# Kernel tuning notes

Measured on AMD Instinct MI355X. Metric: run time of the kernel, lower is better.

## Reference

```python
import jax, jax.numpy as jnp
import numpy as np

V, NJ, NCOMP, NBETA = 778, 16, 24, 10
F_CLOSED, N_ANCHOR = 1554, 32
B, NOBJ = 8, 16384
# MANO kinematic tree parents (wrist + 5 fingers x 3 joints)
PARENTS = np.array([-1, 0, 1, 2, 0, 4, 5, 0, 7, 8, 0, 10, 11, 0, 13, 14])


def setup_inputs() -> dict:
    key = jax.random.key(0)
    ks = jax.random.split(key, 12)
    hand_pose = jax.random.normal(ks[0], (B, 3 + 3 + NCOMP), jnp.float32) * 0.1
    obj_points = jax.random.normal(ks[1], (B, NOBJ, 3), jnp.float32) * 0.1
    hand_beta = jax.random.normal(ks[2], (B, NBETA), jnp.float32) * 0.5
    v_template = jax.random.normal(ks[3], (V, 3), jnp.float32) * 0.05
    shapedirs = jax.random.normal(ks[4], (V, 3, NBETA), jnp.float32) * 0.01
    posedirs = jax.random.normal(ks[5], (V, 3, (NJ - 1) * 9), jnp.float32) * 0.01
    J_regressor = jax.nn.softmax(jax.random.normal(ks[6], (NJ, V), jnp.float32), axis=-1)
    lbs_weights = jax.nn.softmax(jax.random.normal(ks[7], (V, NJ), jnp.float32) * 2.0, axis=-1)
    pca_comps = jax.random.normal(ks[8], (NCOMP, (NJ - 1) * 3), jnp.float32) * 0.1
    anchor_weights = jax.nn.softmax(jax.random.normal(ks[9], (N_ANCHOR, 3), jnp.float32), axis=-1)
    closed_faces = jax.random.randint(ks[10], (F_CLOSED, 3), 0, V, jnp.int32)
    anchor_face_idx = jax.random.randint(ks[11], (N_ANCHOR, 3), 0, V, jnp.int32)
    return dict(hand_pose=hand_pose, obj_points=obj_points, hand_beta=hand_beta,
                v_template=v_template, shapedirs=shapedirs, posedirs=posedirs,
                J_regressor=J_regressor, lbs_weights=lbs_weights, pca_comps=pca_comps,
                anchor_weights=anchor_weights, closed_faces=closed_faces,
                anchor_face_idx=anchor_face_idx)


def rodrigues(r):
    # r: [..., 3] axis-angle -> [..., 3, 3] rotation matrix
    theta = jnp.sqrt(jnp.sum(r * r, axis=-1, keepdims=True) + 1e-16)
    k = r / theta
    c = jnp.cos(theta)[..., None]
    s = jnp.sin(theta)[..., None]
    kx, ky, kz = k[..., 0], k[..., 1], k[..., 2]
    zero = jnp.zeros_like(kx)
    K = jnp.stack([zero, -kz, ky, kz, zero, -kx, -ky, kx, zero], axis=-1)
    K = K.reshape(r.shape[:-1] + (3, 3))
    I = jnp.eye(3, dtype=r.dtype)
    return c * I + s * K + (1.0 - c) * k[..., :, None] * k[..., None, :]


def mano_verts(hand_pose, hand_beta, v_template, shapedirs, posedirs,
               J_regressor, lbs_weights, pca_comps):
    b = hand_pose.shape[0]
    trans = hand_pose[:, :3]
    root = hand_pose[:, 3:6]
    hand45 = hand_pose[:, 6:] @ pca_comps  # PCA -> 45-dim pose (flat_hand_mean: no mean add)
    full = jnp.concatenate([root, hand45], axis=-1).reshape(b, NJ, 3)
    R = rodrigues(full)  # [B,16,3,3]
    v_shaped = v_template + jnp.einsum('vdk,bk->bvd', shapedirs, hand_beta)
    J = jnp.einsum('jv,bvd->bjd', J_regressor, v_shaped)  # [B,16,3]
    pose_feat = (R[:, 1:] - jnp.eye(3, dtype=R.dtype)).reshape(b, (NJ - 1) * 9)
    v_posed = v_shaped + jnp.einsum('vdp,bp->bvd', posedirs, pose_feat)

    def make44(Rj, tj):  # [B,3,3],[B,3] -> [B,4,4]
        T = jnp.zeros((b, 4, 4), R.dtype)
        return T.at[:, :3, :3].set(Rj).at[:, :3, 3].set(tj).at[:, 3, 3].set(1.0)

    Ts = [make44(R[:, 0], J[:, 0])]
    for j in range(1, NJ):  # fixed small kinematic chain
        p = int(PARENTS[j])
        Ts.append(jnp.einsum('bmn,bnk->bmk', Ts[p], make44(R[:, j], J[:, j] - J[:, p])))
    T = jnp.stack(Ts, axis=1)  # [B,16,4,4] global joint transforms
    corr = jnp.einsum('bjmn,bjn->bjm', T[..., :3, :3], J)
    A = T.at[..., :3, 3].add(-corr)  # relative-to-rest transforms
    Tw = jnp.einsum('vj,bjmn->bvmn', lbs_weights, A)  # per-vertex skinning transform
    verts = jnp.einsum('bvmn,bvn->bvm', Tw[..., :3, :3], v_posed) + Tw[..., :3, 3]
    return verts + trans[:, None, :]


def vertex_normals(verts, faces):  # verts [B,V,3], faces [F,3]
    def one(v):
        p0, p1, p2 = v[faces[:, 0]], v[faces[:, 1]], v[faces[:, 2]]
        fn = jnp.cross(p1 - p0, p2 - p0)
        vn = (jnp.zeros_like(v).at[faces[:, 0]].add(fn)
              .at[faces[:, 1]].add(fn).at[faces[:, 2]].add(fn))
        return vn / (jnp.linalg.norm(vn, axis=-1, keepdims=True) + 1e-8)
    return jax.vmap(one)(verts)


def reference(hand_pose, obj_points, hand_beta, v_template, shapedirs, posedirs,
              J_regressor, lbs_weights, pca_comps, anchor_weights,
              closed_faces, anchor_face_idx):
    verts = mano_verts(hand_pose, hand_beta, v_template, shapedirs, posedirs,
                       J_regressor, lbs_weights, pca_comps)  # [B,778,3]
    # get_NN: squared cdist obj->hand + argmin (the memory-bound bottleneck)
    d2 = (jnp.sum(obj_points * obj_points, -1, keepdims=True)
          + jnp.sum(verts * verts, -1)[:, None, :]
          - 2.0 * jnp.einsum('bnd,bvd->bnv', obj_points, verts))  # [B,NOBJ,778]
    nn_idx = jnp.argmin(d2, axis=-1)  # [B,NOBJ]
    nn_dist = jnp.take_along_axis(d2, nn_idx[..., None], axis=-1)[..., 0]
    # contact_map_of_m_to_n
    cmap = 1.0 - 2.0 * (jax.nn.sigmoid(100.0 * nn_dist) - 0.5)
    # inter_penetr_loss: interior obj points (behind nearest hand vertex normal)
    normals = vertex_normals(verts, closed_faces)
    nn_vert = jnp.take_along_axis(verts, nn_idx[..., None], axis=1)
    nn_norm = jnp.take_along_axis(normals, nn_idx[..., None], axis=1)
    interior = jnp.sum((nn_vert - obj_points) * nn_norm, axis=-1) > 0.0
    penetration = jnp.sum(jnp.where(interior, nn_dist, 0.0)) / hand_pose.shape[0]
    # AnchorLayer: barycentric anchor points on the hand surface
    contact_candidates = jnp.einsum('ak,bakd->bad', anchor_weights, verts[:, anchor_face_idx])
    return cmap, penetration, verts, contact_candidates
```

## Files before the change

kernel.cpp:

```cpp
#include <hip/hip_runtime.h>
#include <math.h>

#define NV 778
#define NJ 16
#define NCOMP 24
#define NBETA 10
#define FC 1554
#define NA 32
#define NB 8
#define NOBJ 16384
#define VD (NV*3)
#define BCH 584
#define NVQ 832
#define NG 104
#define NCB 132

__global__ __launch_bounds__(256) void k_blend(
    const float* __restrict__ hp, const float* __restrict__ pca,
    const float* __restrict__ vt, const float* __restrict__ sd,
    const float* __restrict__ pd, const float* __restrict__ beta,
    const float* __restrict__ Jreg,
    float* __restrict__ VP, float* __restrict__ C0, float* __restrict__ C1,
    float* __restrict__ pen)
{
    int bid = blockIdx.x;
    int t = threadIdx.x;
    int wid = t >> 6, lane = t & 63;

    if (bid >= NB*BCH) {
        int o = (bid - NB*BCH)*4 + wid;
        if (o < 528) {
            int jd, k;
            if (o < 48) { jd = o; k = -1; }
            else        { jd = (o-48)/NBETA; k = (o-48)%NBETA; }
            int j = jd/3, d = jd%3;
            const float* jr = Jreg + j*NV;
            float acc = 0.0f;
            for (int v = lane; v < NV; v += 64) {
                float x = (k < 0) ? vt[v*3+d] : sd[(v*3+d)*NBETA + k];
                acc += jr[v] * x;
            }
            #pragma unroll
            for (int off = 32; off; off >>= 1) acc += __shfl_down(acc, off, 64);
            if (lane == 0) { if (k < 0) C0[jd] = acc; else C1[jd*NBETA + k] = acc; }
        }
        return;
    }

    int b = bid / BCH, c = bid % BCH;
    __shared__ float h45[45];
    __shared__ float sR[NJ*9];
    __shared__ float spf[135];

    if (t < 45) {
        float acc = 0.0f;
        #pragma unroll
        for (int k = 0; k < NCOMP; ++k) acc += hp[b*30 + 6 + k] * pca[k*45 + t];
        h45[t] = acc;
    }
    __syncthreads();
    if (t < NJ) {
        float rx, ry, rz;
        if (t == 0) { rx = hp[b*30+3]; ry = hp[b*30+4]; rz = hp[b*30+5]; }
        else        { rx = h45[(t-1)*3]; ry = h45[(t-1)*3+1]; rz = h45[(t-1)*3+2]; }
        float th = sqrtf(rx*rx + ry*ry + rz*rz + 1e-16f);
        float kx = rx/th, ky = ry/th, kz = rz/th;
        float cc = cosf(th), s = sinf(th), o = 1.0f - cc;
        float R[9];
        R[0] = cc + o*kx*kx;     R[1] = -s*kz + o*kx*ky;  R[2] =  s*ky + o*kx*kz;
        R[3] =  s*kz + o*ky*kx;  R[4] = cc + o*ky*ky;     R[5] = -s*kx + o*ky*kz;
        R[6] = -s*ky + o*kz*kx;  R[7] =  s*kx + o*kz*ky;  R[8] = cc + o*kz*kz;
        #pragma unroll
        for (int i = 0; i < 9; ++i) sR[t*9+i] = R[i];
    }
    __syncthreads();
    if (t < 135) {
        int mn = t % 9;
        float d = (mn == 0 || mn == 4 || mn == 8) ? 1.0f : 0.0f;
        spf[t] = sR[9 + t] - d;
    }
    if (bid == 0 && t == 0) *pen = 0.0f;
    __syncthreads();

    int r = c*4 + wid;
    if (r < VD) {
        const float* p  = pd + r * 135;
        float accP = p[lane] * spf[lane] + p[lane+64] * spf[lane+64];
        accP += (lane < 7) ? p[lane+128] * spf[lane+128] : 0.0f;

        float accS = (lane < NBETA) ? sd[r*NBETA + lane] * beta[b*NBETA + lane] : 0.0f;

        #pragma unroll
        for (int off = 32; off; off >>= 1) {
            accP += __shfl_down(accP, off, 64);
            accS += __shfl_down(accS, off, 64);
        }
        if (lane == 0) VP[b*VD + r] = vt[r] + accS + accP;
    }
}

__global__ __launch_bounds__(256) void k_skel2(
    const float* __restrict__ hp, const float* __restrict__ pca,
    const float* __restrict__ beta,
    const float* __restrict__ C0, const float* __restrict__ C1,
    const float* __restrict__ W, const float* __restrict__ VP,
    const int* __restrict__ faces, const float* __restrict__ aw,
    const int* __restrict__ afi,
    float* __restrict__ verts, float4* __restrict__ PK,
    float* __restrict__ NRM, float* __restrict__ contact)
{
    int b = blockIdx.x, t = threadIdx.x;
    __shared__ float h45[45];
    __shared__ float sR[NJ*9];
    __shared__ float sJ[NJ*3];
    __shared__ float4 sA4[NJ*3];
    __shared__ float sv[VD];
    __shared__ float sn[VD];

    if (t < 45) {
        float acc = 0.0f;
        #pragma unroll
        for (int k = 0; k < NCOMP; ++k) acc += hp[b*30 + 6 + k] * pca[k*45 + t];
        h45[t] = acc;
    }
    for (int i = t; i < VD; i += 256) sn[i] = 0.0f;
    if (t < NVQ - NV) PK[b*NVQ + NV + t] = make_float4(0.f, 0.f, 0.f, 1e30f);
    __syncthreads();

    if (t < NJ) {
        float rx, ry, rz;
        if (t == 0) { rx = hp[b*30+3]; ry = hp[b*30+4]; rz = hp[b*30+5]; }
        else        { rx = h45[(t-1)*3]; ry = h45[(t-1)*3+1]; rz = h45[(t-1)*3+2]; }
        float th = sqrtf(rx*rx + ry*ry + rz*rz + 1e-16f);
        float kx = rx/th, ky = ry/th, kz = rz/th;
        float cc = cosf(th), s = sinf(th), o = 1.0f - cc;
        sR[t*9+0] = cc + o*kx*kx;     sR[t*9+1] = -s*kz + o*kx*ky;  sR[t*9+2] =  s*ky + o*kx*kz;
        sR[t*9+3] =  s*kz + o*ky*kx;  sR[t*9+4] = cc + o*ky*ky;     sR[t*9+5] = -s*kx + o*ky*kz;
        sR[t*9+6] = -s*ky + o*kz*kx;  sR[t*9+7] =  s*kx + o*kz*ky;  sR[t*9+8] = cc + o*kz*kz;
    }
    if (t >= 64 && t < 64 + NJ*3) {
        int o = t - 64;
        float acc = C0[o];
        #pragma unroll
        for (int k = 0; k < NBETA; ++k) acc += C1[o*NBETA + k] * beta[b*NBETA + k];
        sJ[o] = acc;
    }
    __syncthreads();

    if (t < 3) {
        const int par[NJ] = {-1,0,1,2,0,4,5,0,7,8,0,10,11,0,13,14};
        int m = t;
        float Tr[NJ][3], Tt[NJ];
        Tr[0][0] = sR[m*3+0]; Tr[0][1] = sR[m*3+1]; Tr[0][2] = sR[m*3+2];
        Tt[0] = sJ[m];
        #pragma unroll
        for (int j = 1; j < NJ; ++j) {
            int p = par[j];
            float t0 = sJ[j*3+0] - sJ[p*3+0];
            float t1 = sJ[j*3+1] - sJ[p*3+1];
            float t2 = sJ[j*3+2] - sJ[p*3+2];
            float a0 = Tr[p][0], a1 = Tr[p][1], a2 = Tr[p][2];
            #pragma unroll
            for (int n = 0; n < 3; ++n)
                Tr[j][n] = a0*sR[j*9+n] + a1*sR[j*9+3+n] + a2*sR[j*9+6+n];
            Tt[j] = a0*t0 + a1*t1 + a2*t2 + Tt[p];
        }
        #pragma unroll
        for (int j = 0; j < NJ; ++j) {
            float corr = Tr[j][0]*sJ[j*3] + Tr[j][1]*sJ[j*3+1] + Tr[j][2]*sJ[j*3+2];
            sA4[j*3 + m] = make_float4(Tr[j][0], Tr[j][1], Tr[j][2], Tt[j] - corr);
        }
    }
    __syncthreads();

    float tx = hp[b*30+0], ty = hp[b*30+1], tz = hp[b*30+2];
    for (int v = t; v < NV; v += 256) {
        float4 r0 = make_float4(0,0,0,0), r1 = make_float4(0,0,0,0), r2 = make_float4(0,0,0,0);
        const float* w = W + v * NJ;
        for (int j = 0; j < NJ; ++j) {
            float wj = w[j];
            float4 A0 = sA4[j*3+0], A1 = sA4[j*3+1], A2 = sA4[j*3+2];
            r0.x += wj*A0.x; r0.y += wj*A0.y; r0.z += wj*A0.z; r0.w += wj*A0.w;
            r1.x += wj*A1.x; r1.y += wj*A1.y; r1.z += wj*A1.z; r1.w += wj*A1.w;
            r2.x += wj*A2.x; r2.y += wj*A2.y; r2.z += wj*A2.z; r2.w += wj*A2.w;
        }
        float px = VP[b*VD + v*3], py = VP[b*VD + v*3+1], pz = VP[b*VD + v*3+2];
        float x = r0.x*px + r0.y*py + r0.z*pz + r0.w + tx;
        float y = r1.x*px + r1.y*py + r1.z*pz + r1.w + ty;
        float z = r2.x*px + r2.y*py + r2.z*pz + r2.w + tz;
        sv[v*3] = x; sv[v*3+1] = y; sv[v*3+2] = z;
        int i = b*NV + v;
        verts[i*3] = x; verts[i*3+1] = y; verts[i*3+2] = z;
        PK[b*NVQ + v] = make_float4(x, y, z, 0.5f*(x*x + y*y + z*z));
    }
    __syncthreads();

    for (int f = t; f < FC; f += 256) {
        int i0 = faces[f*3], i1 = faces[f*3+1], i2 = faces[f*3+2];
        float ax = sv[i1*3+0]-sv[i0*3+0], ay = sv[i1*3+1]-sv[i0*3+1], az = sv[i1*3+2]-sv[i0*3+2];
        float bx = sv[i2*3+0]-sv[i0*3+0], by = sv[i2*3+1]-sv[i0*3+1], bz = sv[i2*3+2]-sv[i0*3+2];
        float cx = ay*bz - az*by, cy = az*bx - ax*bz, cz = ax*by - ay*bx;
        atomicAdd(&sn[i0*3+0], cx); atomicAdd(&sn[i0*3+1], cy); atomicAdd(&sn[i0*3+2], cz);
        atomicAdd(&sn[i1*3+0], cx); atomicAdd(&sn[i1*3+1], cy); atomicAdd(&sn[i1*3+2], cz);
        atomicAdd(&sn[i2*3+0], cx); atomicAdd(&sn[i2*3+1], cy); atomicAdd(&sn[i2*3+2], cz);
    }
    __syncthreads();

    for (int i = t; i < VD; i += 256) NRM[b*VD + i] = sn[i];
    if (t < NA*3) {
        int a = t / 3, d = t % 3;
        float acc = 0.0f;
        #pragma unroll
        for (int k = 0; k < 3; ++k)
            acc += aw[a*3 + k] * sv[afi[a*3 + k]*3 + d];
        contact[b*NA*3 + t] = acc;
    }
}

#define PROC1(vk, vidx) {                                                        \
    float d0 = fmaf(-ox0, (vk).x, (vk).w);                                       \
    d0 = fmaf(-oy0, (vk).y, d0); d0 = fmaf(-oz0, (vk).z, d0);                    \
    if (d0 < s0) { s0 = d0; j0 = (vidx); }                                       \
    float d1 = fmaf(-ox1, (vk).x, (vk).w);                                       \
    d1 = fmaf(-oy1, (vk).y, d1); d1 = fmaf(-oz1, (vk).z, d1);                    \
    if (d1 < s1) { s1 = d1; j1 = (vidx); } }

#define PROC8(buf, gbase) {                                                      \
    PROC1((buf)[0], (gbase)+0); PROC1((buf)[1], (gbase)+1);                      \
    PROC1((buf)[2], (gbase)+2); PROC1((buf)[3], (gbase)+3);                      \
    PROC1((buf)[4], (gbase)+4); PROC1((buf)[5], (gbase)+5);                      \
    PROC1((buf)[6], (gbase)+6); PROC1((buf)[7], (gbase)+7); }

__global__ __launch_bounds__(256) void k_nn(const float* __restrict__ obj,
                                            const float4* __restrict__ PK,
                                            const float* __restrict__ NRM,
                                            float* __restrict__ cmap,
                                            float* __restrict__ pen)
{
    int blk = blockIdx.x;
    int b = blk >> 5;
    int g = blk & 31;
    int t = threadIdx.x, lane = t & 63, wid = t >> 6;

    __shared__ float4 sPK[NVQ];
    __shared__ float wsum[4];

    int n0 = g*512 + t;
    int n1 = n0 + 256;
    const float* o0p = obj + (b*NOBJ + n0)*3;
    const float* o1p = obj + (b*NOBJ + n1)*3;
    float ox0 = o0p[0], oy0 = o0p[1], oz0 = o0p[2];
    float ox1 = o1p[0], oy1 = o1p[1], oz1 = o1p[2];

    for (int i = t; i < NVQ; i += 256) sPK[i] = PK[b*NVQ + i];
    __syncthreads();

    float s0 = 1e30f, s1 = 1e30f;
    int j0 = 0, j1 = 0;
    {
        float4 A[8], B[8];
        #pragma unroll
        for (int k = 0; k < 8; ++k) A[k] = sPK[k];
        for (int gg = 0; gg + 2 <= NG; gg += 2) {
            #pragma unroll
            for (int k = 0; k < 8; ++k) B[k] = sPK[(gg+1)*8 + k];
            PROC8(A, gg*8);
            if (gg + 2 < NG) {
                #pragma unroll
                for (int k = 0; k < 8; ++k) A[k] = sPK[(gg+2)*8 + k];
            }
            PROC8(B, (gg+1)*8);
        }
    }

    int base = b * NV;
    float osq0 = ox0*ox0 + oy0*oy0 + oz0*oz0;
    float d20 = 2.0f * s0 + osq0;
    cmap[b*NOBJ + n0] = 2.0f / (1.0f + __expf(100.0f * d20));
    float4 q0 = sPK[j0];
    float dp0 = (q0.x - ox0)*NRM[(base+j0)*3+0] + (q0.y - oy0)*NRM[(base+j0)*3+1]
              + (q0.z - oz0)*NRM[(base+j0)*3+2];
    float p = (dp0 > 0.0f) ? d20 : 0.0f;

    float osq1 = ox1*ox1 + oy1*oy1 + oz1*oz1;
    float d21 = 2.0f * s1 + osq1;
    cmap[b*NOBJ + n1] = 2.0f / (1.0f + __expf(100.0f * d21));
    float4 q1 = sPK[j1];
    float dp1 = (q1.x - ox1)*NRM[(base+j1)*3+0] + (q1.y - oy1)*NRM[(base+j1)*3+1]
              + (q1.z - oz1)*NRM[(base+j1)*3+2];
    p += (dp1 > 0.0f) ? d21 : 0.0f;

    for (int off = 32; off; off >>= 1) p += __shfl_down(p, off, 64);
    if (lane == 0) wsum[wid] = p;
    __syncthreads();
    if (t == 0) atomicAdd(pen, (wsum[0] + wsum[1] + wsum[2] + wsum[3]) * (1.0f / NB));
}

extern "C" void kernel_launch(void* const* d_in, const int* in_sizes, int n_in,
                              void* d_out, int out_size, void* d_ws, size_t ws_size,
                              hipStream_t stream)
{
    const float* hp    = (const float*)d_in[0];
    const float* obj   = (const float*)d_in[1];
    const float* beta  = (const float*)d_in[2];
    const float* vt    = (const float*)d_in[3];
    const float* sd    = (const float*)d_in[4];
    const float* pd    = (const float*)d_in[5];
    const float* Jreg  = (const float*)d_in[6];
    const float* W     = (const float*)d_in[7];
    const float* pca   = (const float*)d_in[8];
    const float* aw    = (const float*)d_in[9];
    const int*   faces = (const int*)d_in[10];
    const int*   afi   = (const int*)d_in[11];

    float* out     = (float*)d_out;
    float* cmap    = out;
    float* pen     = out + NB*NOBJ;
    float* verts   = out + NB*NOBJ + 1;
    float* contact = out + NB*NOBJ + 1 + NB*NV*3;

    float* ws   = (float*)d_ws;
    float4* PK  = (float4*)ws;
    float* NRM  = ws + NB*NVQ*4;
    float* VP   = NRM + NB*VD;
    float* C0   = VP + NB*VD;
    float* C1   = C0 + 48;

    k_blend<<<NB*BCH + NCB, 256, 0, stream>>>(hp, pca, vt, sd, pd, beta, Jreg,
                                              VP, C0, C1, pen);
    k_skel2<<<NB, 256, 0, stream>>>(hp, pca, beta, C0, C1, W, VP, faces, aw, afi,
                                    verts, PK, NRM, contact);
    k_nn   <<<NB*32, 256, 0, stream>>>(obj, PK, NRM, cmap, pen);
}
```

Before: 147.3 us.

## Fuse skinning and nearest-neighbour kernels with redundant per-block skinning

Merges the per-batch skinning/normals kernel into the nearest-neighbour kernel, so each of the 32 blocks per batch recomputes the skinned vertices and normals directly into shared memory. This removes one kernel launch and the global round-trip for the packed vertex and normal buffers, and it brings the 8-block serial skinning stage out onto all 256 blocks. In exchange the skinning, face-normal atomics and rotation work are duplicated 32 times, and shared memory per block grows, which may lower occupancy. It also vectorizes the skinning weight loads as float4.

```diff
diff --git a/kernel.cpp b/kernel.cpp
--- a/kernel.cpp
+++ b/kernel.cpp
@@ -99,23 +99,50 @@
     }
 }
 
-__global__ __launch_bounds__(256) void k_skel2(
+#define PROC1(vk, vidx) {                                                        \
+    float d0 = fmaf(-ox0, (vk).x, (vk).w);                                       \
+    d0 = fmaf(-oy0, (vk).y, d0); d0 = fmaf(-oz0, (vk).z, d0);                    \
+    if (d0 < s0) { s0 = d0; j0 = (vidx); }                                       \
+    float d1 = fmaf(-ox1, (vk).x, (vk).w);                                       \
+    d1 = fmaf(-oy1, (vk).y, d1); d1 = fmaf(-oz1, (vk).z, d1);                    \
+    if (d1 < s1) { s1 = d1; j1 = (vidx); } }
+
+#define PROC8(buf, gbase) {                                                      \
+    PROC1((buf)[0], (gbase)+0); PROC1((buf)[1], (gbase)+1);                      \
+    PROC1((buf)[2], (gbase)+2); PROC1((buf)[3], (gbase)+3);                      \
+    PROC1((buf)[4], (gbase)+4); PROC1((buf)[5], (gbase)+5);                      \
+    PROC1((buf)[6], (gbase)+6); PROC1((buf)[7], (gbase)+7); }
+
+__global__ __launch_bounds__(256) void k_mega2(
     const float* __restrict__ hp, const float* __restrict__ pca,
     const float* __restrict__ beta,
     const float* __restrict__ C0, const float* __restrict__ C1,
     const float* __restrict__ W, const float* __restrict__ VP,
     const int* __restrict__ faces, const float* __restrict__ aw,
-    const int* __restrict__ afi,
-    float* __restrict__ verts, float4* __restrict__ PK,
-    float* __restrict__ NRM, float* __restrict__ contact)
+    const int* __restrict__ afi, const float* __restrict__ obj,
+    float* __restrict__ verts, float* __restrict__ cmap,
+    float* __restrict__ contact, float* __restrict__ pen)
 {
-    int b = blockIdx.x, t = threadIdx.x;
-    __shared__ float h45[45];
+    int blk = blockIdx.x;
+    int b = blk >> 5;
+    int g = blk & 31;
+    int t = threadIdx.x, lane = t & 63, wid = t >> 6;
+
+    __shared__ float4 sPK[NVQ];
+    __shared__ float sv[VD];
+    __shared__ float sn[VD];
     __shared__ float sR[NJ*9];
     __shared__ float sJ[NJ*3];
     __shared__ float4 sA4[NJ*3];
-    __shared__ float sv[VD];
-    __shared__ float sn[VD];
+    __shared__ float h45[45];
+    __shared__ float wsum[4];
+
+    int n0 = g*512 + t;
+    int n1 = n0 + 256;
+    const float* o0p = obj + (b*NOBJ + n0)*3;
+    const float* o1p = obj + (b*NOBJ + n1)*3;
+    float ox0 = o0p[0], oy0 = o0p[1], oz0 = o0p[2];
+    float ox1 = o1p[0], oy1 = o1p[1], oz1 = o1p[2];
 
     if (t < 45) {
         float acc = 0.0f;
@@ -124,7 +151,7 @@
         h45[t] = acc;
     }
     for (int i = t; i < VD; i += 256) sn[i] = 0.0f;
-    if (t < NVQ - NV) PK[b*NVQ + NV + t] = make_float4(0.f, 0.f, 0.f, 1e30f);
+    if (t < NVQ - NV) sPK[NV + t] = make_float4(0.f, 0.f, 0.f, 1e30f);
     __syncthreads();
 
     if (t < NJ) {
@@ -176,22 +203,30 @@
     float tx = hp[b*30+0], ty = hp[b*30+1], tz = hp[b*30+2];
     for (int v = t; v < NV; v += 256) {
         float4 r0 = make_float4(0,0,0,0), r1 = make_float4(0,0,0,0), r2 = make_float4(0,0,0,0);
-        const float* w = W + v * NJ;
-        for (int j = 0; j < NJ; ++j) {
-            float wj = w[j];
-            float4 A0 = sA4[j*3+0], A1 = sA4[j*3+1], A2 = sA4[j*3+2];
-            r0.x += wj*A0.x; r0.y += wj*A0.y; r0.z += wj*A0.z; r0.w += wj*A0.w;
-            r1.x += wj*A1.x; r1.y += wj*A1.y; r1.z += wj*A1.z; r1.w += wj*A1.w;
-            r2.x += wj*A2.x; r2.y += wj*A2.y; r2.z += wj*A2.z; r2.w += wj*A2.w;
+        const float4* w4 = (const float4*)(W + v * NJ);
+        #pragma unroll
+        for (int q = 0; q < 4; ++q) {
+            float4 wv = w4[q];
+            #pragma unroll
+            for (int jj = 0; jj < 4; ++jj) {
+                int j = q*4 + jj;
+                float wj = (jj==0)?wv.x:(jj==1)?wv.y:(jj==2)?wv.z:wv.w;
+                float4 A0 = sA4[j*3+0], A1 = sA4[j*3+1], A2 = sA4[j*3+2];
+                r0.x += wj*A0.x; r0.y += wj*A0.y; r0.z += wj*A0.z; r0.w += wj*A0.w;
+                r1.x += wj*A1.x; r1.y += wj*A1.y; r1.z += wj*A1.z; r1.w += wj*A1.w;
+                r2.x += wj*A2.x; r2.y += wj*A2.y; r2.z += wj*A2.z; r2.w += wj*A2.w;
+            }
         }
         float px = VP[b*VD + v*3], py = VP[b*VD + v*3+1], pz = VP[b*VD + v*3+2];
         float x = r0.x*px + r0.y*py + r0.z*pz + r0.w + tx;
         float y = r1.x*px + r1.y*py + r1.z*pz + r1.w + ty;
         float z = r2.x*px + r2.y*py + r2.z*pz + r2.w + tz;
         sv[v*3] = x; sv[v*3+1] = y; sv[v*3+2] = z;
-        int i = b*NV + v;
-        verts[i*3] = x; verts[i*3+1] = y; verts[i*3+2] = z;
-        PK[b*NVQ + v] = make_float4(x, y, z, 0.5f*(x*x + y*y + z*z));
+        sPK[v] = make_float4(x, y, z, 0.5f*(x*x + y*y + z*z));
+        if (g == 0) {
+            int i = b*NV + v;
+            verts[i*3] = x; verts[i*3+1] = y; verts[i*3+2] = z;
+        }
     }
     __syncthreads();
 
@@ -206,8 +241,7 @@
     }
     __syncthreads();
 
-    for (int i = t; i < VD; i += 256) NRM[b*VD + i] = sn[i];
-    if (t < NA*3) {
+    if (g == 0 && t < NA*3) {
         int a = t / 3, d = t % 3;
         float acc = 0.0f;
         #pragma unroll
@@ -215,45 +249,6 @@
             acc += aw[a*3 + k] * sv[afi[a*3 + k]*3 + d];
         contact[b*NA*3 + t] = acc;
     }
-}
-
-#define PROC1(vk, vidx) {                                                        \
-    float d0 = fmaf(-ox0, (vk).x, (vk).w);                                       \
-    d0 = fmaf(-oy0, (vk).y, d0); d0 = fmaf(-oz0, (vk).z, d0);                    \
-    if (d0 < s0) { s0 = d0; j0 = (vidx); }                                       \
-    float d1 = fmaf(-ox1, (vk).x, (vk).w);                                       \
-    d1 = fmaf(-oy1, (vk).y, d1); d1 = fmaf(-oz1, (vk).z, d1);                    \
-    if (d1 < s1) { s1 = d1; j1 = (vidx); } }
-
-#define PROC8(buf, gbase) {                                                      \
-    PROC1((buf)[0], (gbase)+0); PROC1((buf)[1], (gbase)+1);                      \
-    PROC1((buf)[2], (gbase)+2); PROC1((buf)[3], (gbase)+3);                      \
-    PROC1((buf)[4], (gbase)+4); PROC1((buf)[5], (gbase)+5);                      \
-    PROC1((buf)[6], (gbase)+6); PROC1((buf)[7], (gbase)+7); }
-
-__global__ __launch_bounds__(256) void k_nn(const float* __restrict__ obj,
-                                            const float4* __restrict__ PK,
-                                            const float* __restrict__ NRM,
-                                            float* __restrict__ cmap,
-                                            float* __restrict__ pen)
-{
-    int blk = blockIdx.x;
-    int b = blk >> 5;
-    int g = blk & 31;
-    int t = threadIdx.x, lane = t & 63, wid = t >> 6;
-
-    __shared__ float4 sPK[NVQ];
-    __shared__ float wsum[4];
-
-    int n0 = g*512 + t;
-    int n1 = n0 + 256;
-    const float* o0p = obj + (b*NOBJ + n0)*3;
-    const float* o1p = obj + (b*NOBJ + n1)*3;
-    float ox0 = o0p[0], oy0 = o0p[1], oz0 = o0p[2];
-    float ox1 = o1p[0], oy1 = o1p[1], oz1 = o1p[2];
-
-    for (int i = t; i < NVQ; i += 256) sPK[i] = PK[b*NVQ + i];
-    __syncthreads();
 
     float s0 = 1e30f, s1 = 1e30f;
     int j0 = 0, j1 = 0;
@@ -273,21 +268,18 @@
         }
     }
 
-    int base = b * NV;
     float osq0 = ox0*ox0 + oy0*oy0 + oz0*oz0;
     float d20 = 2.0f * s0 + osq0;
     cmap[b*NOBJ + n0] = 2.0f / (1.0f + __expf(100.0f * d20));
     float4 q0 = sPK[j0];
-    float dp0 = (q0.x - ox0)*NRM[(base+j0)*3+0] + (q0.y - oy0)*NRM[(base+j0)*3+1]
-              + (q0.z - oz0)*NRM[(base+j0)*3+2];
+    float dp0 = (q0.x - ox0)*sn[j0*3+0] + (q0.y - oy0)*sn[j0*3+1] + (q0.z - oz0)*sn[j0*3+2];
     float p = (dp0 > 0.0f) ? d20 : 0.0f;
 
     float osq1 = ox1*ox1 + oy1*oy1 + oz1*oz1;
     float d21 = 2.0f * s1 + osq1;
     cmap[b*NOBJ + n1] = 2.0f / (1.0f + __expf(100.0f * d21));
     float4 q1 = sPK[j1];
-    float dp1 = (q1.x - ox1)*NRM[(base+j1)*3+0] + (q1.y - oy1)*NRM[(base+j1)*3+1]
-              + (q1.z - oz1)*NRM[(base+j1)*3+2];
+    float dp1 = (q1.x - ox1)*sn[j1*3+0] + (q1.y - oy1)*sn[j1*3+1] + (q1.z - oz1)*sn[j1*3+2];
     p += (dp1 > 0.0f) ? d21 : 0.0f;
 
     for (int off = 32; off; off >>= 1) p += __shfl_down(p, off, 64);
@@ -320,15 +312,12 @@
     float* contact = out + NB*NOBJ + 1 + NB*NV*3;
 
     float* ws   = (float*)d_ws;
-    float4* PK  = (float4*)ws;
-    float* NRM  = ws + NB*NVQ*4;
-    float* VP   = NRM + NB*VD;
+    float* VP   = ws;
     float* C0   = VP + NB*VD;
     float* C1   = C0 + 48;
 
     k_blend<<<NB*BCH + NCB, 256, 0, stream>>>(hp, pca, vt, sd, pd, beta, Jreg,
                                               VP, C0, C1, pen);
-    k_skel2<<<NB, 256, 0, stream>>>(hp, pca, beta, C0, C1, W, VP, faces, aw, afi,
-                                    verts, PK, NRM, contact);
-    k_nn   <<<NB*32, 256, 0, stream>>>(obj, PK, NRM, cmap, pen);
+    k_mega2<<<NB*32, 256, 0, stream>>>(hp, pca, beta, C0, C1, W, VP, faces, aw,
+                                       afi, obj, verts, cmap, contact, pen);
 }
```

Result: faster. 141.7 us (-3.8%).
